# Performance work log

Measured on AMD Instinct MI355X. Metric: run time of the kernel, lower is better.

The kernel has to match this reference:

```python
import jax, jax.numpy as jnp
import numpy as np

B, N, D, R, H = 8192, 256, 6, 3, 32


def setup_inputs() -> dict:
    key = jax.random.key(0)
    ks = jax.random.split(key, 8)
    neighbor_states = jax.random.normal(ks[0], (B, N, D), dtype=jnp.float32)
    neighbor_roles = jax.random.randint(ks[1], (B, N), 0, R, dtype=jnp.int32)
    neighbor_mask = jax.random.randint(ks[2], (B, N), 0, 2, dtype=jnp.int32).astype(jnp.bool_)
    trust_weights = jax.random.uniform(ks[3], (B, N), dtype=jnp.float32)
    # per-role MLP params: Linear(D,H) -> ReLU -> Linear(H,1)
    s1 = 1.0 / np.sqrt(D)
    s2 = 1.0 / np.sqrt(H)
    W1 = jax.random.uniform(ks[4], (R, D, H), minval=-s1, maxval=s1, dtype=jnp.float32)
    b1 = jax.random.uniform(ks[5], (R, H), minval=-s1, maxval=s1, dtype=jnp.float32)
    W2 = jax.random.uniform(ks[6], (R, H), minval=-s2, maxval=s2, dtype=jnp.float32)
    b2 = jax.random.uniform(ks[7], (R,), minval=-s2, maxval=s2, dtype=jnp.float32)
    return {
        "neighbor_states": neighbor_states,
        "neighbor_roles": neighbor_roles,
        "neighbor_mask": neighbor_mask,
        "trust_weights": trust_weights,
        "W1": W1, "b1": b1, "W2": W2, "b2": b2,
    }


def reference(neighbor_states, neighbor_roles, neighbor_mask, trust_weights, W1, b1, W2, b2):
    maskf = neighbor_mask.astype(jnp.float32)          # [B, N]
    tw = trust_weights * maskf                          # [B, N]
    # per-role attention scores, vectorized over roles: [B, R, N]
    h = jax.nn.relu(jnp.einsum('bnd,rdh->brnh', neighbor_states, W1) + b1[None, :, None, :])
    scores = jnp.einsum('brnh,rh->brn', h, W2) + b2[None, :, None]
    role_mask = (neighbor_roles[:, None, :] == jnp.arange(R)[None, :, None]).astype(jnp.float32) * maskf[:, None, :]
    scores = scores * role_mask                         # NOTE: multiplicative masking, as in original
    m = scores.max(axis=2, keepdims=True)
    e = jnp.exp(scores - m) * role_mask
    aw = e / (e.sum(axis=2, keepdims=True) + 1e-8)      # [B, R, N]
    w = aw * tw[:, None, :]
    ws = jnp.clip(w.sum(axis=2, keepdims=True), 1e-8)   # [B, R, 1]
    mf = jnp.einsum('brn,bnd->brd', w, neighbor_states) / ws  # [B, R, D]
    return mf.reshape(mf.shape[0], R * D)               # concat roles along last dim
```

## Files before the change

kernel.cpp:

```cpp
#include <hip/hip_runtime.h>
#include <math.h>

#define NBATCH 8192
#define NNEI 256
#define NROLE 3
#define NHID 32
#define NDIM 6
#define SSTRIDE 12

typedef float v2f __attribute__((ext_vector_type(2)));
typedef unsigned long long ull;

__device__ __forceinline__ void barrier_lds_only() {
  __asm__ __volatile__("" ::: "memory");
  __builtin_amdgcn_s_waitcnt(0xC07F);
  __builtin_amdgcn_s_barrier();
  __asm__ __volatile__("" ::: "memory");
}

__device__ __forceinline__ float mlp_score(const float x0, const float x1,
                                           const float x2, const float x3,
                                           const float x4, const float x5,
                                           const float* __restrict__ w1,
                                           const float* __restrict__ bb,
                                           const float* __restrict__ w2,
                                           const float b2v) {
  const float x[NDIM] = {x0, x1, x2, x3, x4, x5};
  v2f ac0 = {0.f, 0.f}, ac1 = {0.f, 0.f}, ac2 = {0.f, 0.f}, ac3 = {0.f, 0.f};
#pragma unroll
  for (int h = 0; h < NHID; h += 8) {
    v2f a0 = *(const v2f*)(bb + h + 0);
    v2f a1 = *(const v2f*)(bb + h + 2);
    v2f a2 = *(const v2f*)(bb + h + 4);
    v2f a3 = *(const v2f*)(bb + h + 6);
#pragma unroll
    for (int d = 0; d < NDIM; ++d) {
      const float xv = x[d];
      const v2f xv2 = {xv, xv};
      const float* wc = w1 + d * NHID + h;
      a0 += xv2 * (*(const v2f*)(wc + 0));
      a1 += xv2 * (*(const v2f*)(wc + 2));
      a2 += xv2 * (*(const v2f*)(wc + 4));
      a3 += xv2 * (*(const v2f*)(wc + 6));
    }
    a0.x = fmaxf(a0.x, 0.f); a0.y = fmaxf(a0.y, 0.f);
    a1.x = fmaxf(a1.x, 0.f); a1.y = fmaxf(a1.y, 0.f);
    a2.x = fmaxf(a2.x, 0.f); a2.y = fmaxf(a2.y, 0.f);
    a3.x = fmaxf(a3.x, 0.f); a3.y = fmaxf(a3.y, 0.f);
    ac0 += a0 * (*(const v2f*)(w2 + h + 0));
    ac1 += a1 * (*(const v2f*)(w2 + h + 2));
    ac2 += a2 * (*(const v2f*)(w2 + h + 4));
    ac3 += a3 * (*(const v2f*)(w2 + h + 6));
  }
  const v2f st = (ac0 + ac1) + (ac2 + ac3);
  return b2v + st.x + st.y;
}

__global__ __launch_bounds__(256) void hmf_main(
    const float* __restrict__ states,
    const int* __restrict__ roles,
    const int* __restrict__ maskp,
    const float* __restrict__ trust,
    const float* __restrict__ W1,
    const float* __restrict__ b1,
    const float* __restrict__ W2,
    const float* __restrict__ b2g,
    float* __restrict__ out) {
  const int b = blockIdx.x;
  const int tid = threadIdx.x;
  const int wave = tid >> 6;
  const int lane = tid & 63;

  __shared__ float ssort[NNEI * SSTRIDE];
  __shared__ int scnt[12];

  const size_t rowb = (size_t)b * NNEI;
  const int myrole = roles[rowb + tid];
  const int mymask = maskp[rowb + tid];
  const float mytw = trust[rowb + tid];
  const float* sp = states + rowb * NDIM + (size_t)tid * NDIM;
  const float2 sA = *(const float2*)(sp);
  const float2 sB = *(const float2*)(sp + 2);
  const float2 sC = *(const float2*)(sp + 4);
  const bool active = (mymask != 0);

  const ull bal0 = __ballot(active && (myrole == 0));
  const ull bal1 = __ballot(active && (myrole == 1));
  const ull bal2 = __ballot(active && (myrole == 2));
  const int c0 = __popcll(bal0);
  const int c1 = __popcll(bal1);
  const int c2 = __popcll(bal2);
  if (lane < 3) scnt[wave * 3 + lane] = (lane == 0) ? c0 : (lane == 1) ? c1 : c2;

  if (active) {
    const ull mybal = (myrole == 0) ? bal0 : (myrole == 1) ? bal1 : bal2;
    const int rank = __popcll(mybal & ((1ull << lane) - 1ull));
    const int pre = ((myrole >= 1) ? c0 : 0) + ((myrole >= 2) ? c1 : 0);
    const int pos = wave * 64 + pre + rank;
    float* dst = ssort + pos * SSTRIDE;
    *(float4*)dst = make_float4(sA.x, sA.y, sB.x, sB.y);
    *(float2*)(dst + 4) = make_float2(sC.x, sC.y);
    dst[6] = mytw;
  }
  barrier_lds_only();

  if (wave < 3) {
    const int r = __builtin_amdgcn_readfirstlane(wave);
    int cwv[4], prw[4];
#pragma unroll
    for (int w = 0; w < 4; ++w) {
      const int a0 = scnt[w * 3 + 0];
      const int a1 = scnt[w * 3 + 1];
      const int a2 = scnt[w * 3 + 2];
      const int cv = (r == 0) ? a0 : (r == 1) ? a1 : a2;
      const int pv = ((r >= 1) ? a0 : 0) + ((r >= 2) ? a1 : 0);
      cwv[w] = __builtin_amdgcn_readfirstlane(cv);
      prw[w] = __builtin_amdgcn_readfirstlane(pv);
    }
    const int acc0 = cwv[0];
    const int acc1 = acc0 + cwv[1];
    const int acc2 = acc1 + cwv[2];
    const int cnt = acc2 + cwv[3];

    const float* w1 = W1 + r * (NDIM * NHID);
    const float* bb = b1 + r * NHID;
    const float* w2 = W2 + r * NHID;
    const float b2v = b2g[r];

    float q0, q1, q2, q3, q4, q5, q6, q7;

    if (cnt <= 64) {
      const bool act = lane < cnt;
      const bool s1 = lane >= acc0;
      const bool s2 = lane >= acc1;
      const bool s3 = lane >= acc2;
      int sub = s1 ? acc0 : 0; sub = s2 ? acc1 : sub; sub = s3 ? acc2 : sub;
      int wb = s1 ? 64 : 0;    wb = s2 ? 128 : wb;    wb = s3 ? 192 : wb;
      int pr = s1 ? prw[1] : prw[0]; pr = s2 ? prw[2] : pr; pr = s3 ? prw[3] : pr;
      int pos = wb + pr + (lane - sub);
      pos = (pos > NNEI - 1) ? (NNEI - 1) : pos;
      const float* s = ssort + pos * SSTRIDE;
      float4 v4 = *(const float4*)s;
      float2 v2 = *(const float2*)(s + 4);
      float tw = s[6];
      if (!act) {
        v4 = make_float4(0.f, 0.f, 0.f, 0.f);
        v2 = make_float2(0.f, 0.f);
        tw = 0.f;
      }
      const float sc = mlp_score(v4.x, v4.y, v4.z, v4.w, v2.x, v2.y, w1, bb, w2, b2v);
      const float e = act ? __expf(sc) : 0.f;
      const float et = e * tw;
      q0 = e; q1 = et;
      q2 = et * v4.x; q3 = et * v4.y; q4 = et * v4.z;
      q5 = et * v4.w; q6 = et * v2.x; q7 = et * v2.y;
    } else {
      q0 = q1 = q2 = q3 = q4 = q5 = q6 = q7 = 0.f;
      const int nch = (cnt + 63) >> 6;
      for (int c = 0; c < nch; ++c) {
        const int jj = c * 64 + lane;
        const bool act = jj < cnt;
        const bool s1 = jj >= acc0;
        const bool s2 = jj >= acc1;
        const bool s3 = jj >= acc2;
        int sub = s1 ? acc0 : 0; sub = s2 ? acc1 : sub; sub = s3 ? acc2 : sub;
        int wb = s1 ? 64 : 0;    wb = s2 ? 128 : wb;    wb = s3 ? 192 : wb;
        int pr = s1 ? prw[1] : prw[0]; pr = s2 ? prw[2] : pr; pr = s3 ? prw[3] : pr;
        int pos = wb + pr + (jj - sub);
        pos = (pos > NNEI - 1) ? (NNEI - 1) : pos;
        pos = (pos < 0) ? 0 : pos;
        const float* s = ssort + pos * SSTRIDE;
        float4 v4 = *(const float4*)s;
        float2 v2 = *(const float2*)(s + 4);
        float tw = s[6];
        if (!act) {
          v4 = make_float4(0.f, 0.f, 0.f, 0.f);
          v2 = make_float2(0.f, 0.f);
          tw = 0.f;
        }
        const float sc = mlp_score(v4.x, v4.y, v4.z, v4.w, v2.x, v2.y, w1, bb, w2, b2v);
        const float e = act ? __expf(sc) : 0.f;
        const float et = e * tw;
        q0 += e; q1 += et;
        q2 = fmaf(et, v4.x, q2); q3 = fmaf(et, v4.y, q3);
        q4 = fmaf(et, v4.z, q4); q5 = fmaf(et, v4.w, q5);
        q6 = fmaf(et, v2.x, q6); q7 = fmaf(et, v2.y, q7);
      }
    }

#pragma unroll
    for (int off = 1; off <= 4; off <<= 1) {
      q0 += __shfl_xor(q0, off); q1 += __shfl_xor(q1, off);
      q2 += __shfl_xor(q2, off); q3 += __shfl_xor(q3, off);
      q4 += __shfl_xor(q4, off); q5 += __shfl_xor(q5, off);
      q6 += __shfl_xor(q6, off); q7 += __shfl_xor(q7, off);
    }
    const int g = lane & 7;
    float myq = q0;
    myq = (g == 1) ? q1 : myq;
    myq = (g == 2) ? q2 : myq;
    myq = (g == 3) ? q3 : myq;
    myq = (g == 4) ? q4 : myq;
    myq = (g == 5) ? q5 : myq;
    myq = (g == 6) ? q6 : myq;
    myq = (g == 7) ? q7 : myq;
    myq += __shfl_xor(myq, 8);
    myq += __shfl_xor(myq, 16);
    myq += __shfl_xor(myq, 32);
    const float Se = __shfl(myq, 0);
    const float Set = __shfl(myq, 1);
    const float denom = Se + 1e-8f;
    const float ws = fmaxf(Set / denom, 1e-8f);
    if (lane >= 2 && lane < 8) {
      out[(size_t)b * (NROLE * NDIM) + r * NDIM + (lane - 2)] = (myq / denom) / ws;
    }
  }
}

extern "C" void kernel_launch(void* const* d_in, const int* in_sizes, int n_in,
                              void* d_out, int out_size, void* d_ws, size_t ws_size,
                              hipStream_t stream) {
  const float* states = (const float*)d_in[0];
  const int* roles = (const int*)d_in[1];
  const int* maskp = (const int*)d_in[2];
  const float* trust = (const float*)d_in[3];
  const float* W1 = (const float*)d_in[4];
  const float* b1 = (const float*)d_in[5];
  const float* W2 = (const float*)d_in[6];
  const float* b2 = (const float*)d_in[7];
  float* out = (float*)d_out;

  hmf_main<<<NBATCH, 256, 0, stream>>>(states, roles, maskp, trust, W1, b1, W2, b2, out);
}
```

Before: 119.9 us.

## Process each batch row with a single wave instead of a 256-thread block

Restructures the kernel so one 64-lane wave handles a whole batch row. It loads four chunks of neighbours, compacts them by role into LDS using ballots, then loops over the three roles serially. This removes the block barrier and the cross-wave count exchange, and stops one of the four waves from idling during scoring. In exchange, each wave performs all three roles' MLP work in sequence, and the per-wave LDS footprint may limit occupancy.

```diff
diff --git a/kernel.cpp b/kernel.cpp
--- a/kernel.cpp
+++ b/kernel.cpp
@@ -6,17 +6,11 @@
 #define NROLE 3
 #define NHID 32
 #define NDIM 6
+#define NCHUNK 4
 #define SSTRIDE 12
 
 typedef float v2f __attribute__((ext_vector_type(2)));
 typedef unsigned long long ull;
-
-__device__ __forceinline__ void barrier_lds_only() {
-  __asm__ __volatile__("" ::: "memory");
-  __builtin_amdgcn_s_waitcnt(0xC07F);
-  __builtin_amdgcn_s_barrier();
-  __asm__ __volatile__("" ::: "memory");
-}
 
 __device__ __forceinline__ float mlp_score(const float x0, const float x1,
                                            const float x2, const float x3,
@@ -56,7 +50,7 @@
   return b2v + st.x + st.y;
 }
 
-__global__ __launch_bounds__(256) void hmf_main(
+__global__ __launch_bounds__(64, 4) void hmf_wave(
     const float* __restrict__ states,
     const int* __restrict__ roles,
     const int* __restrict__ maskp,
@@ -67,125 +61,92 @@
     const float* __restrict__ b2g,
     float* __restrict__ out) {
   const int b = blockIdx.x;
-  const int tid = threadIdx.x;
-  const int wave = tid >> 6;
-  const int lane = tid & 63;
+  const int lane = threadIdx.x;
 
   __shared__ float ssort[NNEI * SSTRIDE];
-  __shared__ int scnt[12];
 
   const size_t rowb = (size_t)b * NNEI;
-  const int myrole = roles[rowb + tid];
-  const int mymask = maskp[rowb + tid];
-  const float mytw = trust[rowb + tid];
-  const float* sp = states + rowb * NDIM + (size_t)tid * NDIM;
-  const float2 sA = *(const float2*)(sp);
-  const float2 sB = *(const float2*)(sp + 2);
-  const float2 sC = *(const float2*)(sp + 4);
-  const bool active = (mymask != 0);
 
-  const ull bal0 = __ballot(active && (myrole == 0));
-  const ull bal1 = __ballot(active && (myrole == 1));
-  const ull bal2 = __ballot(active && (myrole == 2));
-  const int c0 = __popcll(bal0);
-  const int c1 = __popcll(bal1);
-  const int c2 = __popcll(bal2);
-  if (lane < 3) scnt[wave * 3 + lane] = (lane == 0) ? c0 : (lane == 1) ? c1 : c2;
+  int rl[NCHUNK];
+  int mk[NCHUNK];
+  float tw[NCHUNK];
+  float2 sA[NCHUNK], sB[NCHUNK], sC[NCHUNK];
+#pragma unroll
+  for (int c = 0; c < NCHUNK; ++c) {
+    const size_t idx = rowb + (size_t)(c * 64 + lane);
+    rl[c] = roles[idx];
+    mk[c] = maskp[idx];
+    tw[c] = trust[idx];
+    const float* sp = states + idx * (size_t)NDIM;
+    sA[c] = *(const float2*)(sp);
+    sB[c] = *(const float2*)(sp + 2);
+    sC[c] = *(const float2*)(sp + 4);
+  }
 
-  if (active) {
-    const ull mybal = (myrole == 0) ? bal0 : (myrole == 1) ? bal1 : bal2;
-    const int rank = __popcll(mybal & ((1ull << lane) - 1ull));
-    const int pre = ((myrole >= 1) ? c0 : 0) + ((myrole >= 2) ? c1 : 0);
-    const int pos = wave * 64 + pre + rank;
-    float* dst = ssort + pos * SSTRIDE;
-    *(float4*)dst = make_float4(sA.x, sA.y, sB.x, sB.y);
-    *(float2*)(dst + 4) = make_float2(sC.x, sC.y);
-    dst[6] = mytw;
+  int c0[NCHUNK], c1[NCHUNK], c2[NCHUNK];
+#pragma unroll
+  for (int c = 0; c < NCHUNK; ++c) {
+    const bool a = (mk[c] != 0);
+    c0[c] = __popcll(__ballot(a && rl[c] == 0));
+    c1[c] = __popcll(__ballot(a && rl[c] == 1));
+    c2[c] = __popcll(__ballot(a && rl[c] == 2));
   }
-  barrier_lds_only();
+  const int t0 = c0[0] + c0[1] + c0[2] + c0[3];
+  const int t1 = c1[0] + c1[1] + c1[2] + c1[3];
+  const int t2 = c2[0] + c2[1] + c2[2] + c2[3];
 
-  if (wave < 3) {
-    const int r = __builtin_amdgcn_readfirstlane(wave);
-    int cwv[4], prw[4];
+  int p0 = 0, p1 = 0, p2 = 0;
 #pragma unroll
-    for (int w = 0; w < 4; ++w) {
-      const int a0 = scnt[w * 3 + 0];
-      const int a1 = scnt[w * 3 + 1];
-      const int a2 = scnt[w * 3 + 2];
-      const int cv = (r == 0) ? a0 : (r == 1) ? a1 : a2;
-      const int pv = ((r >= 1) ? a0 : 0) + ((r >= 2) ? a1 : 0);
-      cwv[w] = __builtin_amdgcn_readfirstlane(cv);
-      prw[w] = __builtin_amdgcn_readfirstlane(pv);
+  for (int c = 0; c < NCHUNK; ++c) {
+    const bool a = (mk[c] != 0);
+    const ull balA = __ballot(a && rl[c] == 0);
+    const ull balB = __ballot(a && rl[c] == 1);
+    const ull balC = __ballot(a && rl[c] == 2);
+    if (a) {
+      const int r = rl[c];
+      const ull mybal = (r == 0) ? balA : (r == 1) ? balB : balC;
+      const int rank = __popcll(mybal & ((1ull << lane) - 1ull));
+      const int base = (r == 0) ? 0 : (r == 1) ? t0 : (t0 + t1);
+      const int pre = (r == 0) ? p0 : (r == 1) ? p1 : p2;
+      float* dst = ssort + (size_t)(base + pre + rank) * SSTRIDE;
+      *(float4*)(dst) = make_float4(sA[c].x, sA[c].y, sB[c].x, sB[c].y);
+      *(float4*)(dst + 4) = make_float4(sC[c].x, sC[c].y, tw[c], 0.f);
     }
-    const int acc0 = cwv[0];
-    const int acc1 = acc0 + cwv[1];
-    const int acc2 = acc1 + cwv[2];
-    const int cnt = acc2 + cwv[3];
+    p0 += c0[c];
+    p1 += c1[c];
+    p2 += c2[c];
+  }
 
+  __asm__ __volatile__("s_waitcnt lgkmcnt(0)" ::: "memory");
+
+  const size_t rowo = (size_t)b * (NROLE * NDIM);
+
+#pragma unroll
+  for (int r = 0; r < NROLE; ++r) {
+    const int cr = __builtin_amdgcn_readfirstlane((r == 0) ? t0 : (r == 1) ? t1 : t2);
+    const int br = __builtin_amdgcn_readfirstlane((r == 0) ? 0 : (r == 1) ? t0 : (t0 + t1));
     const float* w1 = W1 + r * (NDIM * NHID);
     const float* bb = b1 + r * NHID;
     const float* w2 = W2 + r * NHID;
     const float b2v = b2g[r];
 
-    float q0, q1, q2, q3, q4, q5, q6, q7;
-
-    if (cnt <= 64) {
-      const bool act = lane < cnt;
-      const bool s1 = lane >= acc0;
-      const bool s2 = lane >= acc1;
-      const bool s3 = lane >= acc2;
-      int sub = s1 ? acc0 : 0; sub = s2 ? acc1 : sub; sub = s3 ? acc2 : sub;
-      int wb = s1 ? 64 : 0;    wb = s2 ? 128 : wb;    wb = s3 ? 192 : wb;
-      int pr = s1 ? prw[1] : prw[0]; pr = s2 ? prw[2] : pr; pr = s3 ? prw[3] : pr;
-      int pos = wb + pr + (lane - sub);
-      pos = (pos > NNEI - 1) ? (NNEI - 1) : pos;
-      const float* s = ssort + pos * SSTRIDE;
-      float4 v4 = *(const float4*)s;
-      float2 v2 = *(const float2*)(s + 4);
-      float tw = s[6];
-      if (!act) {
-        v4 = make_float4(0.f, 0.f, 0.f, 0.f);
-        v2 = make_float2(0.f, 0.f);
-        tw = 0.f;
-      }
-      const float sc = mlp_score(v4.x, v4.y, v4.z, v4.w, v2.x, v2.y, w1, bb, w2, b2v);
-      const float e = act ? __expf(sc) : 0.f;
-      const float et = e * tw;
-      q0 = e; q1 = et;
-      q2 = et * v4.x; q3 = et * v4.y; q4 = et * v4.z;
-      q5 = et * v4.w; q6 = et * v2.x; q7 = et * v2.y;
-    } else {
-      q0 = q1 = q2 = q3 = q4 = q5 = q6 = q7 = 0.f;
-      const int nch = (cnt + 63) >> 6;
-      for (int c = 0; c < nch; ++c) {
-        const int jj = c * 64 + lane;
-        const bool act = jj < cnt;
-        const bool s1 = jj >= acc0;
-        const bool s2 = jj >= acc1;
-        const bool s3 = jj >= acc2;
-        int sub = s1 ? acc0 : 0; sub = s2 ? acc1 : sub; sub = s3 ? acc2 : sub;
-        int wb = s1 ? 64 : 0;    wb = s2 ? 128 : wb;    wb = s3 ? 192 : wb;
-        int pr = s1 ? prw[1] : prw[0]; pr = s2 ? prw[2] : pr; pr = s3 ? prw[3] : pr;
-        int pos = wb + pr + (jj - sub);
-        pos = (pos > NNEI - 1) ? (NNEI - 1) : pos;
-        pos = (pos < 0) ? 0 : pos;
-        const float* s = ssort + pos * SSTRIDE;
-        float4 v4 = *(const float4*)s;
-        float2 v2 = *(const float2*)(s + 4);
-        float tw = s[6];
-        if (!act) {
-          v4 = make_float4(0.f, 0.f, 0.f, 0.f);
-          v2 = make_float2(0.f, 0.f);
-          tw = 0.f;
-        }
-        const float sc = mlp_score(v4.x, v4.y, v4.z, v4.w, v2.x, v2.y, w1, bb, w2, b2v);
-        const float e = act ? __expf(sc) : 0.f;
-        const float et = e * tw;
-        q0 += e; q1 += et;
-        q2 = fmaf(et, v4.x, q2); q3 = fmaf(et, v4.y, q3);
-        q4 = fmaf(et, v4.z, q4); q5 = fmaf(et, v4.w, q5);
-        q6 = fmaf(et, v2.x, q6); q7 = fmaf(et, v2.y, q7);
-      }
+    float q0 = 0.f, q1 = 0.f, q2 = 0.f, q3 = 0.f,
+          q4 = 0.f, q5 = 0.f, q6 = 0.f, q7 = 0.f;
+    for (int j = lane; j < cr; j += 64) {
+      const float* s = ssort + (size_t)(br + j) * SSTRIDE;
+      const float4 v4 = *(const float4*)(s);
+      const float4 vb = *(const float4*)(s + 4);
+      const float sc = mlp_score(v4.x, v4.y, v4.z, v4.w, vb.x, vb.y, w1, bb, w2, b2v);
+      const float e = __expf(sc);
+      const float et = e * vb.z;
+      q0 += e;
+      q1 += et;
+      q2 = fmaf(et, v4.x, q2);
+      q3 = fmaf(et, v4.y, q3);
+      q4 = fmaf(et, v4.z, q4);
+      q5 = fmaf(et, v4.w, q5);
+      q6 = fmaf(et, vb.x, q6);
+      q7 = fmaf(et, vb.y, q7);
     }
 
 #pragma unroll
@@ -212,7 +173,7 @@
     const float denom = Se + 1e-8f;
     const float ws = fmaxf(Set / denom, 1e-8f);
     if (lane >= 2 && lane < 8) {
-      out[(size_t)b * (NROLE * NDIM) + r * NDIM + (lane - 2)] = (myq / denom) / ws;
+      out[rowo + r * NDIM + (lane - 2)] = (myq / denom) / ws;
     }
   }
 }
@@ -230,5 +191,5 @@
   const float* b2 = (const float*)d_in[7];
   float* out = (float*)d_out;
 
-  hmf_main<<<NBATCH, 256, 0, stream>>>(states, roles, maskp, trust, W1, b1, W2, b2, out);
+  hmf_wave<<<NBATCH, 64, 0, stream>>>(states, roles, maskp, trust, W1, b1, W2, b2, out);
 }
```

Result: slower. 148.7 us (+24.1%).

## Stage rows via async global-to-LDS loads, process two batches per 192-thread block

Applied to the files above, without the earlier changes.

The kernel now uses global_load_lds to copy states and trust weights straight into shared memory, replacing the register round-trip and scattered sorted writes. It stores only a permutation index per neighbor and gathers through it. Each block handles two batch rows with three waves, so no wave sits idle after the sort. This adds an extra indirection and possible LDS bank conflicts from the stride-6 gather.

```diff
diff --git a/kernel.cpp b/kernel.cpp
--- a/kernel.cpp
+++ b/kernel.cpp
@@ -6,16 +6,14 @@
 #define NROLE 3
 #define NHID 32
 #define NDIM 6
-#define SSTRIDE 12
 
 typedef float v2f __attribute__((ext_vector_type(2)));
 typedef unsigned long long ull;
 
-__device__ __forceinline__ void barrier_lds_only() {
-  __asm__ __volatile__("" ::: "memory");
-  __builtin_amdgcn_s_waitcnt(0xC07F);
-  __builtin_amdgcn_s_barrier();
-  __asm__ __volatile__("" ::: "memory");
+__device__ __forceinline__ void stage_lds16(const float* g, float* l) {
+  __builtin_amdgcn_global_load_lds(
+      (const __attribute__((address_space(1))) void*)g,
+      (__attribute__((address_space(3))) void*)l, 16, 0, 0);
 }
 
 __device__ __forceinline__ float mlp_score(const float x0, const float x1,
@@ -56,7 +54,29 @@
   return b2v + st.x + st.y;
 }
 
-__global__ __launch_bounds__(256) void hmf_main(
+__device__ __forceinline__ void do_chunk(const int c, const int lane,
+                                         const int rolev, const int maskv,
+                                         int (*perm)[NNEI], int* scnt) {
+  const int q = c >> 2, cc = c & 3;
+  const bool active = (maskv != 0);
+  const ull bal0 = __ballot(active && (rolev == 0));
+  const ull bal1 = __ballot(active && (rolev == 1));
+  const ull bal2 = __ballot(active && (rolev == 2));
+  const int n0 = __popcll(bal0);
+  const int n1 = __popcll(bal1);
+  if (lane < 3) {
+    const int n2 = __popcll(bal2);
+    scnt[q * 12 + cc * 3 + lane] = (lane == 0) ? n0 : (lane == 1) ? n1 : n2;
+  }
+  if (active) {
+    const ull mybal = (rolev == 0) ? bal0 : (rolev == 1) ? bal1 : bal2;
+    const int rank = __popcll(mybal & ((1ull << lane) - 1ull));
+    const int pre = ((rolev >= 1) ? n0 : 0) + ((rolev >= 2) ? n1 : 0);
+    perm[q][cc * 64 + pre + rank] = cc * 64 + lane;
+  }
+}
+
+__global__ __launch_bounds__(192, 8) void hmf_main(
     const float* __restrict__ states,
     const int* __restrict__ roles,
     const int* __restrict__ maskp,
@@ -66,52 +86,65 @@
     const float* __restrict__ W2,
     const float* __restrict__ b2g,
     float* __restrict__ out) {
-  const int b = blockIdx.x;
   const int tid = threadIdx.x;
   const int wave = tid >> 6;
   const int lane = tid & 63;
-
-  __shared__ float ssort[NNEI * SSTRIDE];
-  __shared__ int scnt[12];
-
-  const size_t rowb = (size_t)b * NNEI;
-  const int myrole = roles[rowb + tid];
-  const int mymask = maskp[rowb + tid];
-  const float mytw = trust[rowb + tid];
-  const float* sp = states + rowb * NDIM + (size_t)tid * NDIM;
-  const float2 sA = *(const float2*)(sp);
-  const float2 sB = *(const float2*)(sp + 2);
-  const float2 sC = *(const float2*)(sp + 4);
-  const bool active = (mymask != 0);
-
-  const ull bal0 = __ballot(active && (myrole == 0));
-  const ull bal1 = __ballot(active && (myrole == 1));
-  const ull bal2 = __ballot(active && (myrole == 2));
-  const int c0 = __popcll(bal0);
-  const int c1 = __popcll(bal1);
-  const int c2 = __popcll(bal2);
-  if (lane < 3) scnt[wave * 3 + lane] = (lane == 0) ? c0 : (lane == 1) ? c1 : c2;
-
-  if (active) {
-    const ull mybal = (myrole == 0) ? bal0 : (myrole == 1) ? bal1 : bal2;
-    const int rank = __popcll(mybal & ((1ull << lane) - 1ull));
-    const int pre = ((myrole >= 1) ? c0 : 0) + ((myrole >= 2) ? c1 : 0);
-    const int pos = wave * 64 + pre + rank;
-    float* dst = ssort + pos * SSTRIDE;
-    *(float4*)dst = make_float4(sA.x, sA.y, sB.x, sB.y);
-    *(float2*)(dst + 4) = make_float2(sC.x, sC.y);
-    dst[6] = mytw;
-  }
-  barrier_lds_only();
-
-  if (wave < 3) {
-    const int r = __builtin_amdgcn_readfirstlane(wave);
+  const int b0 = blockIdx.x * 2;
+
+  __shared__ float stg[2][1792];
+  __shared__ int perm[2][NNEI];
+  __shared__ int scnt[24];
+
+  const int cA = wave;
+  const int cB = wave + 3;
+  const int cC = wave + 6;
+  const bool hasC = (wave < 2);
+
+  const size_t giA = (size_t)(b0 + (cA >> 2)) * NNEI + (size_t)((cA & 3) * 64 + lane);
+  const size_t giB = (size_t)(b0 + (cB >> 2)) * NNEI + (size_t)((cB & 3) * 64 + lane);
+  const int rlA = roles[giA];
+  const int mkA = maskp[giA];
+  const int rlB = roles[giB];
+  const int mkB = maskp[giB];
+  int rlC = 0, mkC = 0;
+  if (hasC) {
+    const size_t giC = (size_t)(b0 + (cC >> 2)) * NNEI + (size_t)((cC & 3) * 64 + lane);
+    rlC = roles[giC];
+    mkC = maskp[giC];
+  }
+
+#pragma unroll
+  for (int k = 0; k < 5; ++k) {
+    const int s = wave + k * 3;
+    if (s < 14) {
+      const int q = s / 7, ss = s % 7;
+      const float* g = (ss < 6)
+          ? (states + (size_t)(b0 + q) * (NNEI * NDIM) + (size_t)(ss * 256 + lane * 4))
+          : (trust + (size_t)(b0 + q) * NNEI + (size_t)(lane * 4));
+      stage_lds16(g, &stg[q][ss * 256]);
+    }
+  }
+
+  do_chunk(cA, lane, rlA, mkA, perm, scnt);
+  do_chunk(cB, lane, rlB, mkB, perm, scnt);
+  if (hasC) do_chunk(cC, lane, rlC, mkC, perm, scnt);
+
+  __syncthreads();
+
+  const int r = __builtin_amdgcn_readfirstlane(wave);
+  const float* w1 = W1 + r * (NDIM * NHID);
+  const float* bb = b1 + r * NHID;
+  const float* w2 = W2 + r * NHID;
+  const float b2v = b2g[r];
+
+#pragma unroll
+  for (int q = 0; q < 2; ++q) {
     int cwv[4], prw[4];
 #pragma unroll
     for (int w = 0; w < 4; ++w) {
-      const int a0 = scnt[w * 3 + 0];
-      const int a1 = scnt[w * 3 + 1];
-      const int a2 = scnt[w * 3 + 2];
+      const int a0 = scnt[q * 12 + w * 3 + 0];
+      const int a1 = scnt[q * 12 + w * 3 + 1];
+      const int a2 = scnt[q * 12 + w * 3 + 2];
       const int cv = (r == 0) ? a0 : (r == 1) ? a1 : a2;
       const int pv = ((r >= 1) ? a0 : 0) + ((r >= 2) ? a1 : 0);
       cwv[w] = __builtin_amdgcn_readfirstlane(cv);
@@ -121,11 +154,6 @@
     const int acc1 = acc0 + cwv[1];
     const int acc2 = acc1 + cwv[2];
     const int cnt = acc2 + cwv[3];
-
-    const float* w1 = W1 + r * (NDIM * NHID);
-    const float* bb = b1 + r * NHID;
-    const float* w2 = W2 + r * NHID;
-    const float b2v = b2g[r];
 
     float q0, q1, q2, q3, q4, q5, q6, q7;
 
@@ -139,21 +167,27 @@
       int pr = s1 ? prw[1] : prw[0]; pr = s2 ? prw[2] : pr; pr = s3 ? prw[3] : pr;
       int pos = wb + pr + (lane - sub);
       pos = (pos > NNEI - 1) ? (NNEI - 1) : pos;
-      const float* s = ssort + pos * SSTRIDE;
-      float4 v4 = *(const float4*)s;
-      float2 v2 = *(const float2*)(s + 4);
-      float tw = s[6];
+      pos = (pos < 0) ? 0 : pos;
+      int idx = perm[q][pos];
+      idx = (idx > NNEI - 1) ? (NNEI - 1) : idx;
+      idx = (idx < 0) ? 0 : idx;
+      const float* s = &stg[q][idx * 6];
+      float2 va = *(const float2*)(s);
+      float2 vb2 = *(const float2*)(s + 2);
+      float2 vc = *(const float2*)(s + 4);
+      float tw = stg[q][1536 + idx];
       if (!act) {
-        v4 = make_float4(0.f, 0.f, 0.f, 0.f);
-        v2 = make_float2(0.f, 0.f);
+        va = make_float2(0.f, 0.f);
+        vb2 = make_float2(0.f, 0.f);
+        vc = make_float2(0.f, 0.f);
         tw = 0.f;
       }
-      const float sc = mlp_score(v4.x, v4.y, v4.z, v4.w, v2.x, v2.y, w1, bb, w2, b2v);
+      const float sc = mlp_score(va.x, va.y, vb2.x, vb2.y, vc.x, vc.y, w1, bb, w2, b2v);
       const float e = act ? __expf(sc) : 0.f;
       const float et = e * tw;
       q0 = e; q1 = et;
-      q2 = et * v4.x; q3 = et * v4.y; q4 = et * v4.z;
-      q5 = et * v4.w; q6 = et * v2.x; q7 = et * v2.y;
+      q2 = et * va.x; q3 = et * va.y; q4 = et * vb2.x;
+      q5 = et * vb2.y; q6 = et * vc.x; q7 = et * vc.y;
     } else {
       q0 = q1 = q2 = q3 = q4 = q5 = q6 = q7 = 0.f;
       const int nch = (cnt + 63) >> 6;
@@ -169,22 +203,27 @@
         int pos = wb + pr + (jj - sub);
         pos = (pos > NNEI - 1) ? (NNEI - 1) : pos;
         pos = (pos < 0) ? 0 : pos;
-        const float* s = ssort + pos * SSTRIDE;
-        float4 v4 = *(const float4*)s;
-        float2 v2 = *(const float2*)(s + 4);
-        float tw = s[6];
+        int idx = perm[q][pos];
+        idx = (idx > NNEI - 1) ? (NNEI - 1) : idx;
+        idx = (idx < 0) ? 0 : idx;
+        const float* s = &stg[q][idx * 6];
+        float2 va = *(const float2*)(s);
+        float2 vb2 = *(const float2*)(s + 2);
+        float2 vc = *(const float2*)(s + 4);
+        float tw = stg[q][1536 + idx];
         if (!act) {
-          v4 = make_float4(0.f, 0.f, 0.f, 0.f);
-          v2 = make_float2(0.f, 0.f);
+          va = make_float2(0.f, 0.f);
+          vb2 = make_float2(0.f, 0.f);
+          vc = make_float2(0.f, 0.f);
           tw = 0.f;
         }
-        const float sc = mlp_score(v4.x, v4.y, v4.z, v4.w, v2.x, v2.y, w1, bb, w2, b2v);
+        const float sc = mlp_score(va.x, va.y, vb2.x, vb2.y, vc.x, vc.y, w1, bb, w2, b2v);
         const float e = act ? __expf(sc) : 0.f;
         const float et = e * tw;
         q0 += e; q1 += et;
-        q2 = fmaf(et, v4.x, q2); q3 = fmaf(et, v4.y, q3);
-        q4 = fmaf(et, v4.z, q4); q5 = fmaf(et, v4.w, q5);
-        q6 = fmaf(et, v2.x, q6); q7 = fmaf(et, v2.y, q7);
+        q2 = fmaf(et, va.x, q2); q3 = fmaf(et, va.y, q3);
+        q4 = fmaf(et, vb2.x, q4); q5 = fmaf(et, vb2.y, q5);
+        q6 = fmaf(et, vc.x, q6); q7 = fmaf(et, vc.y, q7);
       }
     }
 
@@ -212,7 +251,8 @@
     const float denom = Se + 1e-8f;
     const float ws = fmaxf(Set / denom, 1e-8f);
     if (lane >= 2 && lane < 8) {
-      out[(size_t)b * (NROLE * NDIM) + r * NDIM + (lane - 2)] = (myq / denom) / ws;
+      out[(size_t)(b0 + q) * (NROLE * NDIM) + r * NDIM + (lane - 2)] =
+          (myq / denom) / ws;
     }
   }
 }
@@ -230,5 +270,5 @@
   const float* b2 = (const float*)d_in[7];
   float* out = (float*)d_out;
 
-  hmf_main<<<NBATCH, 256, 0, stream>>>(states, roles, maskp, trust, W1, b1, W2, b2, out);
-}
+  hmf_main<<<NBATCH / 2, 192, 0, stream>>>(states, roles, maskp, trust, W1, b1, W2, b2, out);
+}
```

New measurement: 123.1 us. 1.03x slower.

## Process four batches per block with register prefetch and double-buffered LDS

Applied to the files above, without the earlier changes.

The kernel now launches 2048 blocks of 192 threads, each handling four batch rows. It prefetches the next row's neighbor data into registers and scatters it into a second LDS buffer while the current row's role MLP pass runs, so only one barrier is needed per row. The LDS layout changes from padded AoS to SoA, and the idle fourth wave is removed by giving wave 0 two chunks. This aims to hide global load latency and cut per-block overhead, but it adds register pressure and puts extra load work on wave 0.

```diff
diff --git a/kernel.cpp b/kernel.cpp
--- a/kernel.cpp
+++ b/kernel.cpp
@@ -6,7 +6,8 @@
 #define NROLE 3
 #define NHID 32
 #define NDIM 6
-#define SSTRIDE 12
+#define NPERS 2048
+#define NBPB 4
 
 typedef float v2f __attribute__((ext_vector_type(2)));
 typedef unsigned long long ull;
@@ -56,7 +57,174 @@
   return b2v + st.x + st.y;
 }
 
-__global__ __launch_bounds__(256) void hmf_main(
+struct ChunkRegs {
+  int rl, mk;
+  float tw;
+  float2 a, b, c;
+};
+
+__device__ __forceinline__ void load_chunk(const float* __restrict__ states,
+                                           const int* __restrict__ roles,
+                                           const int* __restrict__ maskp,
+                                           const float* __restrict__ trust,
+                                           const size_t rowb, const int chunk,
+                                           const int lane, ChunkRegs& r) {
+  const size_t gi = rowb + (size_t)(chunk * 64 + lane);
+  r.rl = roles[gi];
+  r.mk = maskp[gi];
+  r.tw = trust[gi];
+  const float* sp = states + gi * (size_t)NDIM;
+  r.a = *(const float2*)(sp);
+  r.b = *(const float2*)(sp + 2);
+  r.c = *(const float2*)(sp + 4);
+}
+
+__device__ __forceinline__ void scatter_chunk(float* __restrict__ sbuf,
+                                              int* __restrict__ scnt,
+                                              const int chunk, const int lane,
+                                              const ChunkRegs& r) {
+  const bool active = (r.mk != 0);
+  const ull bal0 = __ballot(active && (r.rl == 0));
+  const ull bal1 = __ballot(active && (r.rl == 1));
+  const ull bal2 = __ballot(active && (r.rl == 2));
+  const int n0 = __popcll(bal0);
+  const int n1 = __popcll(bal1);
+  if (lane < 3) {
+    const int n2 = __popcll(bal2);
+    scnt[chunk * 3 + lane] = (lane == 0) ? n0 : (lane == 1) ? n1 : n2;
+  }
+  if (active) {
+    const ull mybal = (r.rl == 0) ? bal0 : (r.rl == 1) ? bal1 : bal2;
+    const int rank = __popcll(mybal & ((1ull << lane) - 1ull));
+    const int pre = ((r.rl >= 1) ? n0 : 0) + ((r.rl >= 2) ? n1 : 0);
+    const int pos = chunk * 64 + pre + rank;
+    sbuf[0 * NNEI + pos] = r.a.x;
+    sbuf[1 * NNEI + pos] = r.a.y;
+    sbuf[2 * NNEI + pos] = r.b.x;
+    sbuf[3 * NNEI + pos] = r.b.y;
+    sbuf[4 * NNEI + pos] = r.c.x;
+    sbuf[5 * NNEI + pos] = r.c.y;
+    sbuf[6 * NNEI + pos] = r.tw;
+  }
+}
+
+__device__ __forceinline__ void role_pass(const float* __restrict__ sbuf,
+                                          const int* __restrict__ scnt,
+                                          const int rw, const int lane,
+                                          const float* __restrict__ w1,
+                                          const float* __restrict__ bb,
+                                          const float* __restrict__ w2,
+                                          const float b2v,
+                                          float* __restrict__ outp) {
+  int cwv[4], prw[4];
+#pragma unroll
+  for (int w = 0; w < 4; ++w) {
+    const int a0 = scnt[w * 3 + 0];
+    const int a1 = scnt[w * 3 + 1];
+    const int a2 = scnt[w * 3 + 2];
+    const int cv = (rw == 0) ? a0 : (rw == 1) ? a1 : a2;
+    const int pv = ((rw >= 1) ? a0 : 0) + ((rw >= 2) ? a1 : 0);
+    cwv[w] = __builtin_amdgcn_readfirstlane(cv);
+    prw[w] = __builtin_amdgcn_readfirstlane(pv);
+  }
+  const int acc0 = cwv[0];
+  const int acc1 = acc0 + cwv[1];
+  const int acc2 = acc1 + cwv[2];
+  const int cnt = acc2 + cwv[3];
+
+  float q0, q1, q2, q3, q4, q5, q6, q7;
+
+  if (cnt <= 64) {
+    const bool act = lane < cnt;
+    const bool s1 = lane >= acc0;
+    const bool s2 = lane >= acc1;
+    const bool s3 = lane >= acc2;
+    int sub = s1 ? acc0 : 0; sub = s2 ? acc1 : sub; sub = s3 ? acc2 : sub;
+    int wb = s1 ? 64 : 0;    wb = s2 ? 128 : wb;    wb = s3 ? 192 : wb;
+    int pr = s1 ? prw[1] : prw[0]; pr = s2 ? prw[2] : pr; pr = s3 ? prw[3] : pr;
+    int pos = wb + pr + (lane - sub);
+    pos = (pos > NNEI - 1) ? (NNEI - 1) : pos;
+    pos = (pos < 0) ? 0 : pos;
+    float x0 = sbuf[0 * NNEI + pos];
+    float x1 = sbuf[1 * NNEI + pos];
+    float x2 = sbuf[2 * NNEI + pos];
+    float x3 = sbuf[3 * NNEI + pos];
+    float x4 = sbuf[4 * NNEI + pos];
+    float x5 = sbuf[5 * NNEI + pos];
+    float tw = sbuf[6 * NNEI + pos];
+    if (!act) {
+      x0 = x1 = x2 = x3 = x4 = x5 = tw = 0.f;
+    }
+    const float sc = mlp_score(x0, x1, x2, x3, x4, x5, w1, bb, w2, b2v);
+    const float e = act ? __expf(sc) : 0.f;
+    const float et = e * tw;
+    q0 = e; q1 = et;
+    q2 = et * x0; q3 = et * x1; q4 = et * x2;
+    q5 = et * x3; q6 = et * x4; q7 = et * x5;
+  } else {
+    q0 = q1 = q2 = q3 = q4 = q5 = q6 = q7 = 0.f;
+    const int nch = (cnt + 63) >> 6;
+    for (int c = 0; c < nch; ++c) {
+      const int jj = c * 64 + lane;
+      const bool act = jj < cnt;
+      const bool s1 = jj >= acc0;
+      const bool s2 = jj >= acc1;
+      const bool s3 = jj >= acc2;
+      int sub = s1 ? acc0 : 0; sub = s2 ? acc1 : sub; sub = s3 ? acc2 : sub;
+      int wb = s1 ? 64 : 0;    wb = s2 ? 128 : wb;    wb = s3 ? 192 : wb;
+      int pr = s1 ? prw[1] : prw[0]; pr = s2 ? prw[2] : pr; pr = s3 ? prw[3] : pr;
+      int pos = wb + pr + (jj - sub);
+      pos = (pos > NNEI - 1) ? (NNEI - 1) : pos;
+      pos = (pos < 0) ? 0 : pos;
+      float x0 = sbuf[0 * NNEI + pos];
+      float x1 = sbuf[1 * NNEI + pos];
+      float x2 = sbuf[2 * NNEI + pos];
+      float x3 = sbuf[3 * NNEI + pos];
+      float x4 = sbuf[4 * NNEI + pos];
+      float x5 = sbuf[5 * NNEI + pos];
+      float tw = sbuf[6 * NNEI + pos];
+      if (!act) {
+        x0 = x1 = x2 = x3 = x4 = x5 = tw = 0.f;
+      }
+      const float sc = mlp_score(x0, x1, x2, x3, x4, x5, w1, bb, w2, b2v);
+      const float e = act ? __expf(sc) : 0.f;
+      const float et = e * tw;
+      q0 += e; q1 += et;
+      q2 = fmaf(et, x0, q2); q3 = fmaf(et, x1, q3);
+      q4 = fmaf(et, x2, q4); q5 = fmaf(et, x3, q5);
+      q6 = fmaf(et, x4, q6); q7 = fmaf(et, x5, q7);
+    }
+  }
+
+#pragma unroll
+  for (int off = 1; off <= 4; off <<= 1) {
+    q0 += __shfl_xor(q0, off); q1 += __shfl_xor(q1, off);
+    q2 += __shfl_xor(q2, off); q3 += __shfl_xor(q3, off);
+    q4 += __shfl_xor(q4, off); q5 += __shfl_xor(q5, off);
+    q6 += __shfl_xor(q6, off); q7 += __shfl_xor(q7, off);
+  }
+  const int g = lane & 7;
+  float myq = q0;
+  myq = (g == 1) ? q1 : myq;
+  myq = (g == 2) ? q2 : myq;
+  myq = (g == 3) ? q3 : myq;
+  myq = (g == 4) ? q4 : myq;
+  myq = (g == 5) ? q5 : myq;
+  myq = (g == 6) ? q6 : myq;
+  myq = (g == 7) ? q7 : myq;
+  myq += __shfl_xor(myq, 8);
+  myq += __shfl_xor(myq, 16);
+  myq += __shfl_xor(myq, 32);
+  const float Se = __shfl(myq, 0);
+  const float Set = __shfl(myq, 1);
+  const float denom = Se + 1e-8f;
+  const float ws = fmaxf(Set / denom, 1e-8f);
+  if (lane >= 2 && lane < 8) {
+    outp[rw * NDIM + (lane - 2)] = (myq / denom) / ws;
+  }
+}
+
+__global__ __launch_bounds__(192, 6) void hmf_main(
     const float* __restrict__ states,
     const int* __restrict__ roles,
     const int* __restrict__ maskp,
@@ -66,153 +234,45 @@
     const float* __restrict__ W2,
     const float* __restrict__ b2g,
     float* __restrict__ out) {
-  const int b = blockIdx.x;
   const int tid = threadIdx.x;
   const int wave = tid >> 6;
   const int lane = tid & 63;
 
-  __shared__ float ssort[NNEI * SSTRIDE];
-  __shared__ int scnt[12];
-
-  const size_t rowb = (size_t)b * NNEI;
-  const int myrole = roles[rowb + tid];
-  const int mymask = maskp[rowb + tid];
-  const float mytw = trust[rowb + tid];
-  const float* sp = states + rowb * NDIM + (size_t)tid * NDIM;
-  const float2 sA = *(const float2*)(sp);
-  const float2 sB = *(const float2*)(sp + 2);
-  const float2 sC = *(const float2*)(sp + 4);
-  const bool active = (mymask != 0);
-
-  const ull bal0 = __ballot(active && (myrole == 0));
-  const ull bal1 = __ballot(active && (myrole == 1));
-  const ull bal2 = __ballot(active && (myrole == 2));
-  const int c0 = __popcll(bal0);
-  const int c1 = __popcll(bal1);
-  const int c2 = __popcll(bal2);
-  if (lane < 3) scnt[wave * 3 + lane] = (lane == 0) ? c0 : (lane == 1) ? c1 : c2;
-
-  if (active) {
-    const ull mybal = (myrole == 0) ? bal0 : (myrole == 1) ? bal1 : bal2;
-    const int rank = __popcll(mybal & ((1ull << lane) - 1ull));
-    const int pre = ((myrole >= 1) ? c0 : 0) + ((myrole >= 2) ? c1 : 0);
-    const int pos = wave * 64 + pre + rank;
-    float* dst = ssort + pos * SSTRIDE;
-    *(float4*)dst = make_float4(sA.x, sA.y, sB.x, sB.y);
-    *(float2*)(dst + 4) = make_float2(sC.x, sC.y);
-    dst[6] = mytw;
-  }
-  barrier_lds_only();
-
-  if (wave < 3) {
-    const int r = __builtin_amdgcn_readfirstlane(wave);
-    int cwv[4], prw[4];
-#pragma unroll
-    for (int w = 0; w < 4; ++w) {
-      const int a0 = scnt[w * 3 + 0];
-      const int a1 = scnt[w * 3 + 1];
-      const int a2 = scnt[w * 3 + 2];
-      const int cv = (r == 0) ? a0 : (r == 1) ? a1 : a2;
-      const int pv = ((r >= 1) ? a0 : 0) + ((r >= 2) ? a1 : 0);
-      cwv[w] = __builtin_amdgcn_readfirstlane(cv);
-      prw[w] = __builtin_amdgcn_readfirstlane(pv);
-    }
-    const int acc0 = cwv[0];
-    const int acc1 = acc0 + cwv[1];
-    const int acc2 = acc1 + cwv[2];
-    const int cnt = acc2 + cwv[3];
-
-    const float* w1 = W1 + r * (NDIM * NHID);
-    const float* bb = b1 + r * NHID;
-    const float* w2 = W2 + r * NHID;
-    const float b2v = b2g[r];
-
-    float q0, q1, q2, q3, q4, q5, q6, q7;
-
-    if (cnt <= 64) {
-      const bool act = lane < cnt;
-      const bool s1 = lane >= acc0;
-      const bool s2 = lane >= acc1;
-      const bool s3 = lane >= acc2;
-      int sub = s1 ? acc0 : 0; sub = s2 ? acc1 : sub; sub = s3 ? acc2 : sub;
-      int wb = s1 ? 64 : 0;    wb = s2 ? 128 : wb;    wb = s3 ? 192 : wb;
-      int pr = s1 ? prw[1] : prw[0]; pr = s2 ? prw[2] : pr; pr = s3 ? prw[3] : pr;
-      int pos = wb + pr + (lane - sub);
-      pos = (pos > NNEI - 1) ? (NNEI - 1) : pos;
-      const float* s = ssort + pos * SSTRIDE;
-      float4 v4 = *(const float4*)s;
-      float2 v2 = *(const float2*)(s + 4);
-      float tw = s[6];
-      if (!act) {
-        v4 = make_float4(0.f, 0.f, 0.f, 0.f);
-        v2 = make_float2(0.f, 0.f);
-        tw = 0.f;
+  __shared__ float soa[2][7 * NNEI];
+  __shared__ int scnt[2][12];
+
+  const int rw = __builtin_amdgcn_readfirstlane(wave);
+  const float* w1 = W1 + rw * (NDIM * NHID);
+  const float* bb = b1 + rw * NHID;
+  const float* w2 = W2 + rw * NHID;
+  const float b2v = b2g[rw];
+  const bool dual = (wave == 0);
+
+  ChunkRegs cr0, cr1;
+  size_t rowb = (size_t)blockIdx.x * NNEI;
+  load_chunk(states, roles, maskp, trust, rowb, wave, lane, cr0);
+  if (dual) load_chunk(states, roles, maskp, trust, rowb, 3, lane, cr1);
+  scatter_chunk(&soa[0][0], scnt[0], wave, lane, cr0);
+  if (dual) scatter_chunk(&soa[0][0], scnt[0], 3, lane, cr1);
+  rowb = (size_t)(blockIdx.x + NPERS) * NNEI;
+  load_chunk(states, roles, maskp, trust, rowb, wave, lane, cr0);
+  if (dual) load_chunk(states, roles, maskp, trust, rowb, 3, lane, cr1);
+
+#pragma unroll
+  for (int t = 0; t < NBPB; ++t) {
+    const int buf = t & 1;
+    barrier_lds_only();
+    const int b = blockIdx.x + t * NPERS;
+    role_pass(&soa[buf][0], scnt[buf], rw, lane, w1, bb, w2, b2v,
+              out + (size_t)b * (NROLE * NDIM));
+    if (t + 1 < NBPB) {
+      scatter_chunk(&soa[buf ^ 1][0], scnt[buf ^ 1], wave, lane, cr0);
+      if (dual) scatter_chunk(&soa[buf ^ 1][0], scnt[buf ^ 1], 3, lane, cr1);
+      if (t + 2 < NBPB) {
+        rowb = (size_t)(blockIdx.x + (t + 2) * NPERS) * NNEI;
+        load_chunk(states, roles, maskp, trust, rowb, wave, lane, cr0);
+        if (dual) load_chunk(states, roles, maskp, trust, rowb, 3, lane, cr1);
       }
-      const float sc = mlp_score(v4.x, v4.y, v4.z, v4.w, v2.x, v2.y, w1, bb, w2, b2v);
-      const float e = act ? __expf(sc) : 0.f;
-      const float et = e * tw;
-      q0 = e; q1 = et;
-      q2 = et * v4.x; q3 = et * v4.y; q4 = et * v4.z;
-      q5 = et * v4.w; q6 = et * v2.x; q7 = et * v2.y;
-    } else {
-      q0 = q1 = q2 = q3 = q4 = q5 = q6 = q7 = 0.f;
-      const int nch = (cnt + 63) >> 6;
-      for (int c = 0; c < nch; ++c) {
-        const int jj = c * 64 + lane;
-        const bool act = jj < cnt;
-        const bool s1 = jj >= acc0;
-        const bool s2 = jj >= acc1;
-        const bool s3 = jj >= acc2;
-        int sub = s1 ? acc0 : 0; sub = s2 ? acc1 : sub; sub = s3 ? acc2 : sub;
-        int wb = s1 ? 64 : 0;    wb = s2 ? 128 : wb;    wb = s3 ? 192 : wb;
-        int pr = s1 ? prw[1] : prw[0]; pr = s2 ? prw[2] : pr; pr = s3 ? prw[3] : pr;
-        int pos = wb + pr + (jj - sub);
-        pos = (pos > NNEI - 1) ? (NNEI - 1) : pos;
-        pos = (pos < 0) ? 0 : pos;
-        const float* s = ssort + pos * SSTRIDE;
-        float4 v4 = *(const float4*)s;
-        float2 v2 = *(const float2*)(s + 4);
-        float tw = s[6];
-        if (!act) {
-          v4 = make_float4(0.f, 0.f, 0.f, 0.f);
-          v2 = make_float2(0.f, 0.f);
-          tw = 0.f;
-        }
-        const float sc = mlp_score(v4.x, v4.y, v4.z, v4.w, v2.x, v2.y, w1, bb, w2, b2v);
-        const float e = act ? __expf(sc) : 0.f;
-        const float et = e * tw;
-        q0 += e; q1 += et;
-        q2 = fmaf(et, v4.x, q2); q3 = fmaf(et, v4.y, q3);
-        q4 = fmaf(et, v4.z, q4); q5 = fmaf(et, v4.w, q5);
-        q6 = fmaf(et, v2.x, q6); q7 = fmaf(et, v2.y, q7);
-      }
-    }
-
-#pragma unroll
-    for (int off = 1; off <= 4; off <<= 1) {
-      q0 += __shfl_xor(q0, off); q1 += __shfl_xor(q1, off);
-      q2 += __shfl_xor(q2, off); q3 += __shfl_xor(q3, off);
-      q4 += __shfl_xor(q4, off); q5 += __shfl_xor(q5, off);
-      q6 += __shfl_xor(q6, off); q7 += __shfl_xor(q7, off);
-    }
-    const int g = lane & 7;
-    float myq = q0;
-    myq = (g == 1) ? q1 : myq;
-    myq = (g == 2) ? q2 : myq;
-    myq = (g == 3) ? q3 : myq;
-    myq = (g == 4) ? q4 : myq;
-    myq = (g == 5) ? q5 : myq;
-    myq = (g == 6) ? q6 : myq;
-    myq = (g == 7) ? q7 : myq;
-    myq += __shfl_xor(myq, 8);
-    myq += __shfl_xor(myq, 16);
-    myq += __shfl_xor(myq, 32);
-    const float Se = __shfl(myq, 0);
-    const float Set = __shfl(myq, 1);
-    const float denom = Se + 1e-8f;
-    const float ws = fmaxf(Set / denom, 1e-8f);
-    if (lane >= 2 && lane < 8) {
-      out[(size_t)b * (NROLE * NDIM) + r * NDIM + (lane - 2)] = (myq / denom) / ws;
     }
   }
 }
@@ -230,5 +290,5 @@
   const float* b2 = (const float*)d_in[7];
   float* out = (float*)d_out;
 
-  hmf_main<<<NBATCH, 256, 0, stream>>>(states, roles, maskp, trust, W1, b1, W2, b2, out);
-}
+  hmf_main<<<NPERS, 192, 0, stream>>>(states, roles, maskp, trust, W1, b1, W2, b2, out);
+}
```

Result: slower. 169.8 us (+41.7%).
